# Kernel tuning notes

Hardware: AMD Instinct MI355X
Metric: run time of the kernel (lower is better)

## Reference

```python
import jax, jax.numpy as jnp
import numpy as np

E = 1024
H = 16
HD = E // H
D = 8  # lattice.d
B, S = 4, 1024


def setup_inputs() -> dict:
    key = jax.random.key(0)
    ks = jax.random.split(key, 9)
    inp = {
        'input_encodings': jax.random.normal(ks[0], (B, S, E, D), dtype=jnp.float32),
        'q_weight_encodings': jax.random.normal(ks[1], (E, E, D), dtype=jnp.float32) * 0.02,
        'k_weight_encodings': jax.random.normal(ks[2], (E, E, D), dtype=jnp.float32) * 0.02,
        'v_weight_encodings': jax.random.normal(ks[3], (E, E, D), dtype=jnp.float32) * 0.02,
        'out_weight_encodings': jax.random.normal(ks[4], (E, E, D), dtype=jnp.float32) * 0.02,
        'q_bias': jax.random.normal(ks[5], (E,), dtype=jnp.float32),
        'k_bias': jax.random.normal(ks[6], (E,), dtype=jnp.float32),
        'v_bias': jax.random.normal(ks[7], (E,), dtype=jnp.float32),
        'out_bias': jax.random.normal(ks[8], (E,), dtype=jnp.float32),
    }
    return inp


def vlut_matmul(x_enc, w_enc):
    # x_enc: [N, E, d] lattice-encoded activations; w_enc: [E, F, d] lattice-encoded weights.
    # vLUT matrix-multiply = sum over channels of encoded inner products.
    return jnp.einsum('ned,efd->nf', x_enc, w_enc)


def reference(input_encodings, q_weight_encodings, k_weight_encodings, v_weight_encodings,
              out_weight_encodings, q_bias, k_bias, v_bias, out_bias):
    b, s, e, d = input_encodings.shape
    x = input_encodings.reshape(b * s, e, d)

    q = vlut_matmul(x, q_weight_encodings) + q_bias
    k = vlut_matmul(x, k_weight_encodings) + k_bias
    v = vlut_matmul(x, v_weight_encodings) + v_bias

    # [B, H, S, HD]
    q = q.reshape(b, s, H, HD).transpose(0, 2, 1, 3)
    k = k.reshape(b, s, H, HD).transpose(0, 2, 1, 3)
    v = v.reshape(b, s, H, HD).transpose(0, 2, 1, 3)

    scale = 1.0 / np.sqrt(HD).astype(np.float32)
    attn_scores = jnp.einsum('bhqd,bhkd->bhqk', q, k) * scale
    attn_weights = jax.nn.softmax(attn_scores, axis=-1)
    attn_output = jnp.einsum('bhqk,bhkd->bhqd', attn_weights, v)
    attn_output = attn_output.transpose(0, 2, 1, 3).reshape(b * s, e)

    # output vLUT projection (broadcast interpretation over lattice dim d)
    output = jnp.einsum('ne,efd->nf', attn_output, out_weight_encodings)
    output = output.reshape(b, s, e) + out_bias
    return output, attn_weights
```

## Files before the change

### kernel.cpp

```cpp
#include <hip/hip_runtime.h>

typedef _Float16 f16;
typedef f16 f16x8 __attribute__((ext_vector_type(8)));
typedef float f32x4 __attribute__((ext_vector_type(4)));

#define NTOK 4096
#define EDIM 1024
#define KQKV 8192
#define SEQ  1024
#define HD   64

__device__ __forceinline__ float dot4(f32x4 a, f32x4 b) {
  return a[0]*b[0] + a[1]*b[1] + a[2]*b[2] + a[3]*b[3];
}

__device__ __forceinline__ void gl16(const void* g, void* l) {
  __builtin_amdgcn_global_load_lds(
      (const __attribute__((address_space(1))) void*)g,
      (__attribute__((address_space(3))) void*)l, 16, 0, 0);
}

__global__ void k_split(const float* __restrict__ in, f16* __restrict__ hi,
                        f16* __restrict__ lo, int n8) {
  int stride = gridDim.x * blockDim.x;
  for (int i = blockIdx.x * blockDim.x + threadIdx.x; i < n8; i += stride) {
    const float4* p = (const float4*)in + (size_t)i * 2;
    float4 a = p[0], b = p[1];
    float v[8] = {a.x, a.y, a.z, a.w, b.x, b.y, b.z, b.w};
    f16x8 h, l;
#pragma unroll
    for (int j = 0; j < 8; j++) {
      f16 hv = (f16)v[j];
      h[j] = hv;
      l[j] = (f16)(v[j] - (float)hv);
    }
    ((f16x8*)hi)[i] = h;
    ((f16x8*)lo)[i] = l;
  }
}

__global__ void k_wsumt(const float* __restrict__ wout, float* __restrict__ wsumT) {
  __shared__ float tile[32][65];
  int e0 = blockIdx.x * 32, f0 = blockIdx.y * 64;
  int t = threadIdx.x;
#pragma unroll
  for (int rep = 0; rep < 8; rep++) {
    int idx = rep * 256 + t;
    int el = idx >> 6, fl = idx & 63;
    const float* p = wout + ((size_t)(e0 + el) * 1024 + (f0 + fl)) * 8;
    float4 r0 = *(const float4*)p, r1 = *(const float4*)(p + 4);
    tile[el][fl] = r0.x + r0.y + r0.z + r0.w + r1.x + r1.y + r1.z + r1.w;
  }
  __syncthreads();
#pragma unroll
  for (int rep = 0; rep < 8; rep++) {
    int idx = rep * 256 + t;
    int fl = idx >> 5, el = idx & 31;
    wsumT[(size_t)(f0 + fl) * 1024 + (e0 + el)] = tile[el][fl];
  }
}

__global__ __launch_bounds__(256, 2)
void k_gemm_qkv(const f16* __restrict__ xhi, const f16* __restrict__ xlo,
                const f16* __restrict__ wqh, const f16* __restrict__ wql,
                const f16* __restrict__ wkh, const f16* __restrict__ wkl,
                const f16* __restrict__ wvh, const f16* __restrict__ wvl,
                const float* __restrict__ qb, const float* __restrict__ kb,
                const float* __restrict__ vb,
                float* __restrict__ Q, float* __restrict__ K, float* __restrict__ V) {
  __shared__ __align__(16) f16 lAh[4096];
  __shared__ __align__(16) f16 lAl[4096];
  __shared__ __align__(16) f16 lBh[4096];
  __shared__ __align__(16) f16 lBl[4096];

  int z = blockIdx.z;
  const f16* bh_ = z == 0 ? wqh : (z == 1 ? wkh : wvh);
  const f16* bl_ = z == 0 ? wql : (z == 1 ? wkl : wvl);
  const float* bias = z == 0 ? qb : (z == 1 ? kb : vb);
  float* out = z == 0 ? Q : (z == 1 ? K : V);

  int t = threadIdx.x;
  int wave = t >> 6, lane = t & 63;
  int lr = lane & 15, lk = lane >> 4;
  int wr = wave >> 1, wc = wave & 1;
  int rowblk = blockIdx.x * 128, colblk = blockIdx.y * 128;

  {
  }
  int arow = t >> 2, acs = t & 3;
  int agc = acs ^ ((arow >> 1) & 3);
  const f16* pAh = xhi + (size_t)(rowblk + arow) * KQKV + (agc << 3);
  const f16* pAl = xlo + (size_t)(rowblk + arow) * KQKV + (agc << 3);
  const f16* pBh = bh_ + (size_t)(t >> 7) * 8192 + ((size_t)colblk + (t & 127)) * 8;
  const f16* pBl = bl_ + (size_t)(t >> 7) * 8192 + ((size_t)colblk + (t & 127)) * 8;

  f16* dAh0 = lAh + t * 8;            f16* dAh1 = lAh + (t + 256) * 8;
  f16* dAl0 = lAl + t * 8;            f16* dAl1 = lAl + (t + 256) * 8;
  f16* dBh0 = lBh + t * 8;            f16* dBh1 = lBh + (t + 256) * 8;
  f16* dBl0 = lBl + t * 8;            f16* dBl1 = lBl + (t + 256) * 8;

  int aswz = (lk ^ ((lr >> 1) & 3)) << 3;
  int aidx[4];
#pragma unroll
  for (int m = 0; m < 4; m++) aidx[m] = (wr * 64 + m * 16 + lr) * 32 + aswz;
  int bidx[4];
#pragma unroll
  for (int n = 0; n < 4; n++) bidx[n] = (lk * 128 + wc * 64 + n * 16 + lr) << 3;

  f32x4 acc[4][4] = {};

  for (int kt = 0; kt < KQKV / 32; ++kt) {
    gl16(pAh, dAh0);  gl16(pAh + 64 * KQKV, dAh1);
    gl16(pAl, dAl0);  gl16(pAl + 64 * KQKV, dAl1);
    gl16(pBh, dBh0);  gl16(pBh + 2 * 8192, dBh1);
    gl16(pBl, dBl0);  gl16(pBl + 2 * 8192, dBl1);
    pAh += 32; pAl += 32; pBh += 4 * 8192; pBl += 4 * 8192;

    __syncthreads();

    f16x8 ah[4], al[4], bh[4], bl[4];
#pragma unroll
    for (int m = 0; m < 4; m++) {
      ah[m] = *(const f16x8*)&lAh[aidx[m]];
      al[m] = *(const f16x8*)&lAl[aidx[m]];
    }
#pragma unroll
    for (int n = 0; n < 4; n++) {
      bh[n] = *(const f16x8*)&lBh[bidx[n]];
      bl[n] = *(const f16x8*)&lBl[bidx[n]];
    }
#pragma unroll
    for (int m = 0; m < 4; m++)
#pragma unroll
      for (int n = 0; n < 4; n++) {
        acc[m][n] = __builtin_amdgcn_mfma_f32_16x16x32_f16(ah[m], bh[n], acc[m][n], 0, 0, 0);
        acc[m][n] = __builtin_amdgcn_mfma_f32_16x16x32_f16(ah[m], bl[n], acc[m][n], 0, 0, 0);
        acc[m][n] = __builtin_amdgcn_mfma_f32_16x16x32_f16(al[m], bh[n], acc[m][n], 0, 0, 0);
      }

    __syncthreads();
  }

  int row0 = rowblk + wr * 64, col0 = colblk + wc * 64;
  float bv[4];
#pragma unroll
  for (int n = 0; n < 4; n++) bv[n] = bias[col0 + n * 16 + lr];
#pragma unroll
  for (int m = 0; m < 4; m++) {
    int r0 = row0 + m * 16 + lk * 4;
#pragma unroll
    for (int n = 0; n < 4; n++) {
      int c = col0 + n * 16 + lr;
      float* dst = out + (size_t)r0 * EDIM + c;
#pragma unroll
      for (int i = 0; i < 4; i++)
        dst[(size_t)i * EDIM] = acc[m][n][i] + bv[n];
    }
  }
}

__global__ __launch_bounds__(256)
void k_scores(const float* __restrict__ Q, const float* __restrict__ K,
              float* __restrict__ attn) {
  __shared__ float Qt[64][68];
  __shared__ float Kt[64][68];
  int z = blockIdx.z;
  int b = z >> 4, h = z & 15;
  int q0 = blockIdx.x * 64, k0 = blockIdx.y * 64;
  int t = threadIdx.x;
  size_t qbase = ((size_t)(b * SEQ + q0)) * EDIM + h * HD;
  size_t kbase = ((size_t)(b * SEQ + k0)) * EDIM + h * HD;
#pragma unroll
  for (int rep = 0; rep < 4; rep++) {
    int idx = rep * 256 + t;
    int r = idx >> 4, c4 = (idx & 15) * 4;
    *(f32x4*)&Qt[r][c4] = *(const f32x4*)(Q + qbase + (size_t)r * EDIM + c4);
    *(f32x4*)&Kt[r][c4] = *(const f32x4*)(K + kbase + (size_t)r * EDIM + c4);
  }
  __syncthreads();
  int tq = t >> 4, tk = t & 15;
  float acc[4][4] = {};
  for (int c0 = 0; c0 < 64; c0 += 4) {
    f32x4 a4[4], b4[4];
#pragma unroll
    for (int i = 0; i < 4; i++) a4[i] = *(const f32x4*)&Qt[tq + 16 * i][c0];
#pragma unroll
    for (int j = 0; j < 4; j++) b4[j] = *(const f32x4*)&Kt[tk + 16 * j][c0];
#pragma unroll
    for (int i = 0; i < 4; i++)
#pragma unroll
      for (int j = 0; j < 4; j++)
        acc[i][j] += dot4(a4[i], b4[j]);
  }
  const float scale = 0.125f;
  float* dst = attn + ((size_t)z * SEQ + q0) * SEQ + k0;
#pragma unroll
  for (int i = 0; i < 4; i++)
#pragma unroll
    for (int j = 0; j < 4; j++)
      dst[(size_t)(tq + 16 * i) * SEQ + tk + 16 * j] = acc[i][j] * scale;
}

__global__ __launch_bounds__(256)
void k_softmax(float* __restrict__ attn) {
  __shared__ float red[8];
  size_t row = blockIdx.x;
  float* p = attn + row * 1024;
  int t = threadIdx.x;
  float4 v = *(float4*)(p + t * 4);
  float m = fmaxf(fmaxf(v.x, v.y), fmaxf(v.z, v.w));
#pragma unroll
  for (int off = 1; off < 64; off <<= 1) m = fmaxf(m, __shfl_xor(m, off));
  int wv = t >> 6;
  if ((t & 63) == 0) red[wv] = m;
  __syncthreads();
  m = fmaxf(fmaxf(red[0], red[1]), fmaxf(red[2], red[3]));
  float4 e;
  e.x = __expf(v.x - m); e.y = __expf(v.y - m);
  e.z = __expf(v.z - m); e.w = __expf(v.w - m);
  float s = e.x + e.y + e.z + e.w;
#pragma unroll
  for (int off = 1; off < 64; off <<= 1) s += __shfl_xor(s, off);
  if ((t & 63) == 0) red[4 + wv] = s;
  __syncthreads();
  s = red[4] + red[5] + red[6] + red[7];
  float inv = 1.0f / s;
  v.x = e.x * inv; v.y = e.y * inv; v.z = e.z * inv; v.w = e.w * inv;
  *(float4*)(p + t * 4) = v;
}

__global__ __launch_bounds__(256)
void k_pv(const float* __restrict__ attn, const float* __restrict__ V,
          float* __restrict__ aout) {
  __shared__ float Wt[64][68];
  __shared__ float VtT[64][68];
  int z = blockIdx.y;
  int b = z >> 4, h = z & 15;
  int s0 = blockIdx.x * 64;
  int t = threadIdx.x;
  int tq = t >> 4, th = t & 15;
  float acc[4][4] = {};
  for (int k0 = 0; k0 < SEQ; k0 += 64) {
    __syncthreads();
#pragma unroll
    for (int rep = 0; rep < 4; rep++) {
      int idx = rep * 256 + t;
      int r = idx >> 4, c4 = (idx & 15) * 4;
      *(f32x4*)&Wt[r][c4] =
          *(const f32x4*)(attn + ((size_t)z * SEQ + s0 + r) * SEQ + k0 + c4);
      f32x4 vv = *(const f32x4*)(V + ((size_t)(b * SEQ + k0 + r)) * EDIM + h * HD + c4);
#pragma unroll
      for (int c = 0; c < 4; c++) VtT[c4 + c][r] = vv[c];
    }
    __syncthreads();
    for (int c0 = 0; c0 < 64; c0 += 4) {
      f32x4 a4[4], b4[4];
#pragma unroll
      for (int i = 0; i < 4; i++) a4[i] = *(const f32x4*)&Wt[tq + 16 * i][c0];
#pragma unroll
      for (int j = 0; j < 4; j++) b4[j] = *(const f32x4*)&VtT[th + 16 * j][c0];
#pragma unroll
      for (int i = 0; i < 4; i++)
#pragma unroll
        for (int j = 0; j < 4; j++)
          acc[i][j] += dot4(a4[i], b4[j]);
    }
  }
#pragma unroll
  for (int i = 0; i < 4; i++)
#pragma unroll
    for (int j = 0; j < 4; j++)
      aout[((size_t)(b * SEQ + s0 + tq + 16 * i)) * EDIM + h * HD + th + 16 * j] =
          acc[i][j];
}

__global__ __launch_bounds__(256)
void k_outproj(const float* __restrict__ A, const float* __restrict__ BT,
               const float* __restrict__ bias, float* __restrict__ outp) {
  __shared__ float At[64][68];
  __shared__ float Bt[64][68];
  int n0 = blockIdx.x * 64, f0 = blockIdx.y * 64;
  int t = threadIdx.x;
  int tn = t >> 4, tf = t & 15;
  float acc[4][4] = {};
  for (int e0 = 0; e0 < EDIM; e0 += 64) {
    __syncthreads();
#pragma unroll
    for (int rep = 0; rep < 4; rep++) {
      int idx = rep * 256 + t;
      int r = idx >> 4, c4 = (idx & 15) * 4;
      *(f32x4*)&At[r][c4] = *(const f32x4*)(A + (size_t)(n0 + r) * EDIM + e0 + c4);
      *(f32x4*)&Bt[r][c4] = *(const f32x4*)(BT + (size_t)(f0 + r) * EDIM + e0 + c4);
    }
    __syncthreads();
    for (int c0 = 0; c0 < 64; c0 += 4) {
      f32x4 a4[4], b4[4];
#pragma unroll
      for (int i = 0; i < 4; i++) a4[i] = *(const f32x4*)&At[tn + 16 * i][c0];
#pragma unroll
      for (int j = 0; j < 4; j++) b4[j] = *(const f32x4*)&Bt[tf + 16 * j][c0];
#pragma unroll
      for (int i = 0; i < 4; i++)
#pragma unroll
        for (int j = 0; j < 4; j++)
          acc[i][j] += dot4(a4[i], b4[j]);
    }
  }
#pragma unroll
  for (int i = 0; i < 4; i++)
#pragma unroll
    for (int j = 0; j < 4; j++)
      outp[(size_t)(n0 + tn + 16 * i) * EDIM + f0 + tf + 16 * j] =
          acc[i][j] + bias[f0 + tf + 16 * j];
}

extern "C" void kernel_launch(void* const* d_in, const int* in_sizes, int n_in,
                              void* d_out, int out_size, void* d_ws, size_t ws_size,
                              hipStream_t stream) {
  const float* x  = (const float*)d_in[0];
  const float* wq = (const float*)d_in[1];
  const float* wk = (const float*)d_in[2];
  const float* wv = (const float*)d_in[3];
  const float* wo = (const float*)d_in[4];
  const float* qb = (const float*)d_in[5];
  const float* kb = (const float*)d_in[6];
  const float* vb = (const float*)d_in[7];
  const float* ob = (const float*)d_in[8];

  float* outp = (float*)d_out;
  float* attn = outp + (size_t)4 * 1024 * 1024;

  char* w = (char*)d_ws;
  f16* xhi = (f16*)w;  w += (size_t)33554432 * 2;
  f16* xlo = (f16*)w;  w += (size_t)33554432 * 2;
  f16* wqh = (f16*)w;  w += (size_t)8388608 * 2;
  f16* wql = (f16*)w;  w += (size_t)8388608 * 2;
  f16* wkh = (f16*)w;  w += (size_t)8388608 * 2;
  f16* wkl = (f16*)w;  w += (size_t)8388608 * 2;
  f16* wvh = (f16*)w;  w += (size_t)8388608 * 2;
  f16* wvl = (f16*)w;  w += (size_t)8388608 * 2;
  float* Q    = (float*)w; w += (size_t)4194304 * 4;
  float* K    = (float*)w; w += (size_t)4194304 * 4;
  float* V    = (float*)w; w += (size_t)4194304 * 4;
  float* aout = (float*)w; w += (size_t)4194304 * 4;
  float* wsumT = (float*)w; w += (size_t)1048576 * 4;

  k_split<<<8192, 256, 0, stream>>>(x, xhi, xlo, 4194304);
  k_split<<<4096, 256, 0, stream>>>(wq, wqh, wql, 1048576);
  k_split<<<4096, 256, 0, stream>>>(wk, wkh, wkl, 1048576);
  k_split<<<4096, 256, 0, stream>>>(wv, wvh, wvl, 1048576);
  k_wsumt<<<dim3(32, 16), 256, 0, stream>>>(wo, wsumT);
  k_gemm_qkv<<<dim3(32, 8, 3), 256, 0, stream>>>(xhi, xlo, wqh, wql, wkh, wkl,
                                                 wvh, wvl, qb, kb, vb, Q, K, V);
  k_scores<<<dim3(16, 16, 64), 256, 0, stream>>>(Q, K, attn);
  k_softmax<<<65536, 256, 0, stream>>>(attn);
  k_pv<<<dim3(16, 64), 256, 0, stream>>>(attn, V, aout);
  k_outproj<<<dim3(64, 16), 256, 0, stream>>>(aout, wsumT, ob, outp);
}
```

Before: 1.681 ms.

## Fuse scores, softmax and PV into one MFMA attention kernel; MFMA out-projection

Measured after the change: 1.445 ms. 1.16x faster.

```diff
diff --git a/kernel.cpp b/kernel.cpp
--- a/kernel.cpp
+++ b/kernel.cpp
@@ -4,15 +4,10 @@
 typedef f16 f16x8 __attribute__((ext_vector_type(8)));
 typedef float f32x4 __attribute__((ext_vector_type(4)));
 
-#define NTOK 4096
 #define EDIM 1024
 #define KQKV 8192
 #define SEQ  1024
 #define HD   64
-
-__device__ __forceinline__ float dot4(f32x4 a, f32x4 b) {
-  return a[0]*b[0] + a[1]*b[1] + a[2]*b[2] + a[3]*b[3];
-}
 
 __device__ __forceinline__ void gl16(const void* g, void* l) {
   __builtin_amdgcn_global_load_lds(
@@ -39,7 +34,8 @@
   }
 }
 
-__global__ void k_wsumt(const float* __restrict__ wout, float* __restrict__ wsumT) {
+__global__ void k_wsumt(const float* __restrict__ wout, f16* __restrict__ wth,
+                        f16* __restrict__ wtl) {
   __shared__ float tile[32][65];
   int e0 = blockIdx.x * 32, f0 = blockIdx.y * 64;
   int t = threadIdx.x;
@@ -56,7 +52,11 @@
   for (int rep = 0; rep < 8; rep++) {
     int idx = rep * 256 + t;
     int fl = idx >> 5, el = idx & 31;
-    wsumT[(size_t)(f0 + fl) * 1024 + (e0 + el)] = tile[el][fl];
+    float v = tile[el][fl];
+    f16 h = (f16)v;
+    size_t o = (size_t)(f0 + fl) * 1024 + e0 + el;
+    wth[o] = h;
+    wtl[o] = (f16)(v - (float)h);
   }
 }
 
@@ -73,7 +73,7 @@
   __shared__ __align__(16) f16 lBh[4096];
   __shared__ __align__(16) f16 lBl[4096];
 
-  int z = blockIdx.z;
+  int z = blockIdx.y;
   const f16* bh_ = z == 0 ? wqh : (z == 1 ? wkh : wvh);
   const f16* bl_ = z == 0 ? wql : (z == 1 ? wkl : wvl);
   const float* bias = z == 0 ? qb : (z == 1 ? kb : vb);
@@ -83,10 +83,8 @@
   int wave = t >> 6, lane = t & 63;
   int lr = lane & 15, lk = lane >> 4;
   int wr = wave >> 1, wc = wave & 1;
-  int rowblk = blockIdx.x * 128, colblk = blockIdx.y * 128;
-
-  {
-  }
+  int rowblk = blockIdx.z * 128, colblk = blockIdx.x * 128;
+
   int arow = t >> 2, acs = t & 3;
   int agc = acs ^ ((arow >> 1) & 3);
   const f16* pAh = xhi + (size_t)(rowblk + arow) * KQKV + (agc << 3);
@@ -94,10 +92,10 @@
   const f16* pBh = bh_ + (size_t)(t >> 7) * 8192 + ((size_t)colblk + (t & 127)) * 8;
   const f16* pBl = bl_ + (size_t)(t >> 7) * 8192 + ((size_t)colblk + (t & 127)) * 8;
 
-  f16* dAh0 = lAh + t * 8;            f16* dAh1 = lAh + (t + 256) * 8;
-  f16* dAl0 = lAl + t * 8;            f16* dAl1 = lAl + (t + 256) * 8;
-  f16* dBh0 = lBh + t * 8;            f16* dBh1 = lBh + (t + 256) * 8;
-  f16* dBl0 = lBl + t * 8;            f16* dBl1 = lBl + (t + 256) * 8;
+  f16* dAh0 = lAh + t * 8;  f16* dAh1 = lAh + (t + 256) * 8;
+  f16* dAl0 = lAl + t * 8;  f16* dAl1 = lAl + (t + 256) * 8;
+  f16* dBh0 = lBh + t * 8;  f16* dBh1 = lBh + (t + 256) * 8;
+  f16* dBl0 = lBl + t * 8;  f16* dBl1 = lBl + (t + 256) * 8;
 
   int aswz = (lk ^ ((lr >> 1) & 3)) << 3;
   int aidx[4];
@@ -159,159 +157,312 @@
   }
 }
 
+__device__ __forceinline__ void stage_tile64(const float* __restrict__ src,
+                                             f16* __restrict__ dh, f16* __restrict__ dl,
+                                             int sr, int sc4) {
+  const float* p = src + (size_t)sr * EDIM + sc4;
+  float4 v0 = *(const float4*)p;
+  float4 v1 = *(const float4*)(p + 4);
+  float4 v2 = *(const float4*)(p + 8);
+  float4 v3 = *(const float4*)(p + 12);
+  float vv[16] = {v0.x, v0.y, v0.z, v0.w, v1.x, v1.y, v1.z, v1.w,
+                  v2.x, v2.y, v2.z, v2.w, v3.x, v3.y, v3.z, v3.w};
+  f16x8 ha, la, hb, lb;
+#pragma unroll
+  for (int j = 0; j < 8; j++) {
+    f16 x = (f16)vv[j];
+    ha[j] = x; la[j] = (f16)(vv[j] - (float)x);
+    f16 y = (f16)vv[8 + j];
+    hb[j] = y; lb[j] = (f16)(vv[8 + j] - (float)y);
+  }
+  int c0 = sc4 >> 3;
+  int ca = ((c0 ^ (sr & 7)) << 3), cb = (((c0 + 1) ^ (sr & 7)) << 3);
+  *(f16x8*)&dh[sr * 64 + ca] = ha;
+  *(f16x8*)&dl[sr * 64 + ca] = la;
+  *(f16x8*)&dh[sr * 64 + cb] = hb;
+  *(f16x8*)&dl[sr * 64 + cb] = lb;
+}
+
+__device__ __forceinline__ void stage_vt(const float* __restrict__ src,
+                                         f16* __restrict__ dh, f16* __restrict__ dl,
+                                         int sr, int sc4) {
+  const float* p = src + (size_t)sr * EDIM + sc4;
+  float4 v0 = *(const float4*)p;
+  float4 v1 = *(const float4*)(p + 4);
+  float4 v2 = *(const float4*)(p + 8);
+  float4 v3 = *(const float4*)(p + 12);
+  float vv[16] = {v0.x, v0.y, v0.z, v0.w, v1.x, v1.y, v1.z, v1.w,
+                  v2.x, v2.y, v2.z, v2.w, v3.x, v3.y, v3.z, v3.w};
+#pragma unroll
+  for (int j = 0; j < 16; j++) {
+    int hd = sc4 + j;
+    f16 x = (f16)vv[j];
+    int off = hd * 64 + (((sr >> 3) ^ (hd & 7)) << 3) + (sr & 7);
+    dh[off] = x;
+    dl[off] = (f16)(vv[j] - (float)x);
+  }
+}
+
 __global__ __launch_bounds__(256)
-void k_scores(const float* __restrict__ Q, const float* __restrict__ K,
-              float* __restrict__ attn) {
-  __shared__ float Qt[64][68];
-  __shared__ float Kt[64][68];
-  int z = blockIdx.z;
-  int b = z >> 4, h = z & 15;
-  int q0 = blockIdx.x * 64, k0 = blockIdx.y * 64;
-  int t = threadIdx.x;
-  size_t qbase = ((size_t)(b * SEQ + q0)) * EDIM + h * HD;
-  size_t kbase = ((size_t)(b * SEQ + k0)) * EDIM + h * HD;
-#pragma unroll
-  for (int rep = 0; rep < 4; rep++) {
-    int idx = rep * 256 + t;
-    int r = idx >> 4, c4 = (idx & 15) * 4;
-    *(f32x4*)&Qt[r][c4] = *(const f32x4*)(Q + qbase + (size_t)r * EDIM + c4);
-    *(f32x4*)&Kt[r][c4] = *(const f32x4*)(K + kbase + (size_t)r * EDIM + c4);
-  }
-  __syncthreads();
-  int tq = t >> 4, tk = t & 15;
-  float acc[4][4] = {};
-  for (int c0 = 0; c0 < 64; c0 += 4) {
-    f32x4 a4[4], b4[4];
-#pragma unroll
-    for (int i = 0; i < 4; i++) a4[i] = *(const f32x4*)&Qt[tq + 16 * i][c0];
-#pragma unroll
-    for (int j = 0; j < 4; j++) b4[j] = *(const f32x4*)&Kt[tk + 16 * j][c0];
-#pragma unroll
-    for (int i = 0; i < 4; i++)
-#pragma unroll
-      for (int j = 0; j < 4; j++)
-        acc[i][j] += dot4(a4[i], b4[j]);
-  }
-  const float scale = 0.125f;
-  float* dst = attn + ((size_t)z * SEQ + q0) * SEQ + k0;
-#pragma unroll
-  for (int i = 0; i < 4; i++)
-#pragma unroll
-    for (int j = 0; j < 4; j++)
-      dst[(size_t)(tq + 16 * i) * SEQ + tk + 16 * j] = acc[i][j] * scale;
-}
-
-__global__ __launch_bounds__(256)
-void k_softmax(float* __restrict__ attn) {
-  __shared__ float red[8];
-  size_t row = blockIdx.x;
-  float* p = attn + row * 1024;
-  int t = threadIdx.x;
-  float4 v = *(float4*)(p + t * 4);
-  float m = fmaxf(fmaxf(v.x, v.y), fmaxf(v.z, v.w));
-#pragma unroll
-  for (int off = 1; off < 64; off <<= 1) m = fmaxf(m, __shfl_xor(m, off));
-  int wv = t >> 6;
-  if ((t & 63) == 0) red[wv] = m;
-  __syncthreads();
-  m = fmaxf(fmaxf(red[0], red[1]), fmaxf(red[2], red[3]));
-  float4 e;
-  e.x = __expf(v.x - m); e.y = __expf(v.y - m);
-  e.z = __expf(v.z - m); e.w = __expf(v.w - m);
-  float s = e.x + e.y + e.z + e.w;
-#pragma unroll
-  for (int off = 1; off < 64; off <<= 1) s += __shfl_xor(s, off);
-  if ((t & 63) == 0) red[4 + wv] = s;
-  __syncthreads();
-  s = red[4] + red[5] + red[6] + red[7];
-  float inv = 1.0f / s;
-  v.x = e.x * inv; v.y = e.y * inv; v.z = e.z * inv; v.w = e.w * inv;
-  *(float4*)(p + t * 4) = v;
-}
-
-__global__ __launch_bounds__(256)
-void k_pv(const float* __restrict__ attn, const float* __restrict__ V,
-          float* __restrict__ aout) {
-  __shared__ float Wt[64][68];
-  __shared__ float VtT[64][68];
+void k_attn(const float* __restrict__ Qm, const float* __restrict__ Km,
+            const float* __restrict__ Vm, float* __restrict__ attn,
+            f16* __restrict__ aoh, f16* __restrict__ aol) {
+  __shared__ __align__(16) f16 lKh[4096], lKl[4096];
+  __shared__ __align__(16) f16 lVh[4096], lVl[4096];
+  __shared__ __align__(16) f16 lP[4096];
+  __shared__ float sred[4][64], ssum[4][64];
+  __shared__ float m_run[64], l_run[64], linv[64];
+
   int z = blockIdx.y;
   int b = z >> 4, h = z & 15;
-  int s0 = blockIdx.x * 64;
+  int q0 = blockIdx.x * 64;
   int t = threadIdx.x;
-  int tq = t >> 4, th = t & 15;
-  float acc[4][4] = {};
-  for (int k0 = 0; k0 < SEQ; k0 += 64) {
-    __syncthreads();
-#pragma unroll
-    for (int rep = 0; rep < 4; rep++) {
-      int idx = rep * 256 + t;
-      int r = idx >> 4, c4 = (idx & 15) * 4;
-      *(f32x4*)&Wt[r][c4] =
-          *(const f32x4*)(attn + ((size_t)z * SEQ + s0 + r) * SEQ + k0 + c4);
-      f32x4 vv = *(const f32x4*)(V + ((size_t)(b * SEQ + k0 + r)) * EDIM + h * HD + c4);
-#pragma unroll
-      for (int c = 0; c < 4; c++) VtT[c4 + c][r] = vv[c];
-    }
-    __syncthreads();
-    for (int c0 = 0; c0 < 64; c0 += 4) {
-      f32x4 a4[4], b4[4];
-#pragma unroll
-      for (int i = 0; i < 4; i++) a4[i] = *(const f32x4*)&Wt[tq + 16 * i][c0];
-#pragma unroll
-      for (int j = 0; j < 4; j++) b4[j] = *(const f32x4*)&VtT[th + 16 * j][c0];
+  int w = t >> 6, lane = t & 63, lr = lane & 15, lk = lane >> 4;
+
+  size_t qoff = ((size_t)b * SEQ + q0) * EDIM + h * HD;
+  size_t koff = ((size_t)b * SEQ) * EDIM + h * HD;
+  size_t abase = ((size_t)z * SEQ + q0) * SEQ;
+
+  int sr = t >> 2, sc4 = (t & 3) * 16;
+
+  stage_tile64(Qm + qoff, lKh, lKl, sr, sc4);
+  __syncthreads();
+  f16x8 qh[4][2], ql[4][2];
+#pragma unroll
+  for (int m = 0; m < 4; m++)
+#pragma unroll
+    for (int kk = 0; kk < 2; kk++) {
+      int r = m * 16 + lr;
+      int ch = (((kk * 4 + lk) ^ (r & 7)) << 3);
+      qh[m][kk] = *(const f16x8*)&lKh[r * 64 + ch];
+      ql[m][kk] = *(const f16x8*)&lKl[r * 64 + ch];
+    }
+  if (t < 64) { m_run[t] = -1e30f; l_run[t] = 0.f; }
+  __syncthreads();
+
+  for (int kt = 0; kt < 16; kt++) {
+    stage_tile64(Km + koff + (size_t)(kt * 64) * EDIM, lKh, lKl, sr, sc4);
+    __syncthreads();
+
+    f16x8 kbh[2], kbl[2];
+#pragma unroll
+    for (int kk = 0; kk < 2; kk++) {
+      int r = w * 16 + lr;
+      int ch = (((kk * 4 + lk) ^ (r & 7)) << 3);
+      kbh[kk] = *(const f16x8*)&lKh[r * 64 + ch];
+      kbl[kk] = *(const f16x8*)&lKl[r * 64 + ch];
+    }
+    f32x4 acc[4] = {};
+#pragma unroll
+    for (int m = 0; m < 4; m++)
+#pragma unroll
+      for (int kk = 0; kk < 2; kk++) {
+        acc[m] = __builtin_amdgcn_mfma_f32_16x16x32_f16(qh[m][kk], kbh[kk], acc[m], 0, 0, 0);
+        acc[m] = __builtin_amdgcn_mfma_f32_16x16x32_f16(qh[m][kk], kbl[kk], acc[m], 0, 0, 0);
+        acc[m] = __builtin_amdgcn_mfma_f32_16x16x32_f16(ql[m][kk], kbh[kk], acc[m], 0, 0, 0);
+      }
+
+    float sv[4][4], rm[4][4];
+#pragma unroll
+    for (int m = 0; m < 4; m++)
+#pragma unroll
+      for (int i = 0; i < 4; i++) { sv[m][i] = acc[m][i] * 0.125f; rm[m][i] = sv[m][i]; }
+#pragma unroll
+    for (int off = 1; off < 16; off <<= 1)
+#pragma unroll
+      for (int m = 0; m < 4; m++)
+#pragma unroll
+        for (int i = 0; i < 4; i++)
+          rm[m][i] = fmaxf(rm[m][i], __shfl_xor(rm[m][i], off));
+    if (lr == 0) {
+#pragma unroll
+      for (int m = 0; m < 4; m++)
+#pragma unroll
+        for (int i = 0; i < 4; i++) sred[w][m * 16 + lk * 4 + i] = rm[m][i];
+    }
+    __syncthreads();
+    if (t < 64) {
+      float tm = fmaxf(fmaxf(sred[0][t], sred[1][t]), fmaxf(sred[2][t], sred[3][t]));
+      float mn = fmaxf(m_run[t], tm);
+      sred[0][t] = __expf(m_run[t] - mn);
+      m_run[t] = mn;
+    }
+    __syncthreads();
+#pragma unroll
+    for (int m = 0; m < 4; m++)
 #pragma unroll
       for (int i = 0; i < 4; i++)
-#pragma unroll
-        for (int j = 0; j < 4; j++)
-          acc[i][j] += dot4(a4[i], b4[j]);
-    }
-  }
-#pragma unroll
-  for (int i = 0; i < 4; i++)
-#pragma unroll
-    for (int j = 0; j < 4; j++)
-      aout[((size_t)(b * SEQ + s0 + tq + 16 * i)) * EDIM + h * HD + th + 16 * j] =
-          acc[i][j];
-}
-
-__global__ __launch_bounds__(256)
-void k_outproj(const float* __restrict__ A, const float* __restrict__ BT,
+        sv[m][i] = __expf(sv[m][i] - m_run[m * 16 + lk * 4 + i]);
+#pragma unroll
+    for (int off = 1; off < 16; off <<= 1)
+#pragma unroll
+      for (int m = 0; m < 4; m++)
+#pragma unroll
+        for (int i = 0; i < 4; i++)
+          sv[m][i] += __shfl_xor(sv[m][i], off);
+    if (lr == 0) {
+#pragma unroll
+      for (int m = 0; m < 4; m++)
+#pragma unroll
+        for (int i = 0; i < 4; i++) ssum[w][m * 16 + lk * 4 + i] = sv[m][i];
+    }
+    __syncthreads();
+    if (t < 64)
+      l_run[t] = l_run[t] * sred[0][t] +
+                 (ssum[0][t] + ssum[1][t] + ssum[2][t] + ssum[3][t]);
+    __syncthreads();
+  }
+  if (t < 64) linv[t] = 1.0f / l_run[t];
+  __syncthreads();
+
+  f32x4 acc_o[4] = {};
+  for (int kt = 0; kt < 16; kt++) {
+    stage_tile64(Km + koff + (size_t)(kt * 64) * EDIM, lKh, lKl, sr, sc4);
+    stage_vt(Vm + koff + (size_t)(kt * 64) * EDIM, lVh, lVl, sr, sc4);
+    __syncthreads();
+
+    f16x8 kbh[2], kbl[2];
+#pragma unroll
+    for (int kk = 0; kk < 2; kk++) {
+      int r = w * 16 + lr;
+      int ch = (((kk * 4 + lk) ^ (r & 7)) << 3);
+      kbh[kk] = *(const f16x8*)&lKh[r * 64 + ch];
+      kbl[kk] = *(const f16x8*)&lKl[r * 64 + ch];
+    }
+    f32x4 acc[4] = {};
+#pragma unroll
+    for (int m = 0; m < 4; m++)
+#pragma unroll
+      for (int kk = 0; kk < 2; kk++) {
+        acc[m] = __builtin_amdgcn_mfma_f32_16x16x32_f16(qh[m][kk], kbh[kk], acc[m], 0, 0, 0);
+        acc[m] = __builtin_amdgcn_mfma_f32_16x16x32_f16(qh[m][kk], kbl[kk], acc[m], 0, 0, 0);
+        acc[m] = __builtin_amdgcn_mfma_f32_16x16x32_f16(ql[m][kk], kbh[kk], acc[m], 0, 0, 0);
+      }
+
+#pragma unroll
+    for (int m = 0; m < 4; m++)
+#pragma unroll
+      for (int i = 0; i < 4; i++) {
+        int row = m * 16 + lk * 4 + i;
+        float pr = __expf(acc[m][i] * 0.125f - m_run[row]) * linv[row];
+        attn[abase + (size_t)row * SEQ + kt * 64 + w * 16 + lr] = pr;
+        int key = w * 16 + lr;
+        lP[row * 64 + (((key >> 3) ^ (row & 7)) << 3) + (key & 7)] = (f16)pr;
+      }
+    __syncthreads();
+
+#pragma unroll
+    for (int kk = 0; kk < 2; kk++) {
+      int rv = w * 16 + lr;
+      int chv = (((kk * 4 + lk) ^ (rv & 7)) << 3);
+      f16x8 vbh = *(const f16x8*)&lVh[rv * 64 + chv];
+      f16x8 vbl = *(const f16x8*)&lVl[rv * 64 + chv];
+#pragma unroll
+      for (int m = 0; m < 4; m++) {
+        int rp = m * 16 + lr;
+        int chp = (((kk * 4 + lk) ^ (rp & 7)) << 3);
+        f16x8 pa = *(const f16x8*)&lP[rp * 64 + chp];
+        acc_o[m] = __builtin_amdgcn_mfma_f32_16x16x32_f16(pa, vbh, acc_o[m], 0, 0, 0);
+        acc_o[m] = __builtin_amdgcn_mfma_f32_16x16x32_f16(pa, vbl, acc_o[m], 0, 0, 0);
+      }
+    }
+    __syncthreads();
+  }
+
+  size_t obase = ((size_t)b * SEQ + q0) * EDIM + h * HD + w * 16 + lr;
+#pragma unroll
+  for (int m = 0; m < 4; m++)
+#pragma unroll
+    for (int i = 0; i < 4; i++) {
+      int row = m * 16 + lk * 4 + i;
+      float v = acc_o[m][i];
+      f16 hh = (f16)v;
+      aoh[obase + (size_t)row * EDIM] = hh;
+      aol[obase + (size_t)row * EDIM] = (f16)(v - (float)hh);
+    }
+}
+
+__global__ __launch_bounds__(256, 2)
+void k_outproj(const f16* __restrict__ aoh, const f16* __restrict__ aol,
+               const f16* __restrict__ wth, const f16* __restrict__ wtl,
                const float* __restrict__ bias, float* __restrict__ outp) {
-  __shared__ float At[64][68];
-  __shared__ float Bt[64][68];
-  int n0 = blockIdx.x * 64, f0 = blockIdx.y * 64;
+  __shared__ __align__(16) f16 lAh[4096], lAl[4096], lBh[4096], lBl[4096];
+
   int t = threadIdx.x;
-  int tn = t >> 4, tf = t & 15;
-  float acc[4][4] = {};
-  for (int e0 = 0; e0 < EDIM; e0 += 64) {
-    __syncthreads();
-#pragma unroll
-    for (int rep = 0; rep < 4; rep++) {
-      int idx = rep * 256 + t;
-      int r = idx >> 4, c4 = (idx & 15) * 4;
-      *(f32x4*)&At[r][c4] = *(const f32x4*)(A + (size_t)(n0 + r) * EDIM + e0 + c4);
-      *(f32x4*)&Bt[r][c4] = *(const f32x4*)(BT + (size_t)(f0 + r) * EDIM + e0 + c4);
-    }
-    __syncthreads();
-    for (int c0 = 0; c0 < 64; c0 += 4) {
-      f32x4 a4[4], b4[4];
-#pragma unroll
-      for (int i = 0; i < 4; i++) a4[i] = *(const f32x4*)&At[tn + 16 * i][c0];
-#pragma unroll
-      for (int j = 0; j < 4; j++) b4[j] = *(const f32x4*)&Bt[tf + 16 * j][c0];
+  int wave = t >> 6, lane = t & 63;
+  int lr = lane & 15, lk = lane >> 4;
+  int wr = wave >> 1, wc = wave & 1;
+  int rowblk = blockIdx.y * 128, colblk = blockIdx.x * 128;
+
+  int arow = t >> 2, acs = t & 3;
+  int agc = acs ^ ((arow >> 1) & 3);
+  const f16* pAh = aoh + (size_t)(rowblk + arow) * EDIM + (agc << 3);
+  const f16* pAl = aol + (size_t)(rowblk + arow) * EDIM + (agc << 3);
+  const f16* pBh = wth + (size_t)(colblk + arow) * EDIM + (agc << 3);
+  const f16* pBl = wtl + (size_t)(colblk + arow) * EDIM + (agc << 3);
+
+  f16* dAh0 = lAh + t * 8;  f16* dAh1 = lAh + (t + 256) * 8;
+  f16* dAl0 = lAl + t * 8;  f16* dAl1 = lAl + (t + 256) * 8;
+  f16* dBh0 = lBh + t * 8;  f16* dBh1 = lBh + (t + 256) * 8;
+  f16* dBl0 = lBl + t * 8;  f16* dBl1 = lBl + (t + 256) * 8;
+
+  int aswz = (lk ^ ((lr >> 1) & 3)) << 3;
+  int aidx[4], bidx[4];
+#pragma unroll
+  for (int m = 0; m < 4; m++) aidx[m] = (wr * 64 + m * 16 + lr) * 32 + aswz;
+#pragma unroll
+  for (int n = 0; n < 4; n++) bidx[n] = (wc * 64 + n * 16 + lr) * 32 + aswz;
+
+  f32x4 acc[4][4] = {};
+
+  for (int kt = 0; kt < 32; ++kt) {
+    gl16(pAh, dAh0);  gl16(pAh + 64 * EDIM, dAh1);
+    gl16(pAl, dAl0);  gl16(pAl + 64 * EDIM, dAl1);
+    gl16(pBh, dBh0);  gl16(pBh + 64 * EDIM, dBh1);
+    gl16(pBl, dBl0);  gl16(pBl + 64 * EDIM, dBl1);
+    pAh += 32; pAl += 32; pBh += 32; pBl += 32;
+
+    __syncthreads();
+
+    f16x8 ah[4], al[4], bh[4], bl[4];
+#pragma unroll
+    for (int m = 0; m < 4; m++) {
+      ah[m] = *(const f16x8*)&lAh[aidx[m]];
+      al[m] = *(const f16x8*)&lAl[aidx[m]];
+    }
+#pragma unroll
+    for (int n = 0; n < 4; n++) {
+      bh[n] = *(const f16x8*)&lBh[bidx[n]];
+      bl[n] = *(const f16x8*)&lBl[bidx[n]];
+    }
+#pragma unroll
+    for (int m = 0; m < 4; m++)
+#pragma unroll
+      for (int n = 0; n < 4; n++) {
+        acc[m][n] = __builtin_amdgcn_mfma_f32_16x16x32_f16(ah[m], bh[n], acc[m][n], 0, 0, 0);
+        acc[m][n] = __builtin_amdgcn_mfma_f32_16x16x32_f16(ah[m], bl[n], acc[m][n], 0, 0, 0);
+        acc[m][n] = __builtin_amdgcn_mfma_f32_16x16x32_f16(al[m], bh[n], acc[m][n], 0, 0, 0);
+      }
+
+    __syncthreads();
+  }
+
+  int row0 = rowblk + wr * 64, col0 = colblk + wc * 64;
+  float bv[4];
+#pragma unroll
+  for (int n = 0; n < 4; n++) bv[n] = bias[col0 + n * 16 + lr];
+#pragma unroll
+  for (int m = 0; m < 4; m++) {
+    int r0 = row0 + m * 16 + lk * 4;
+#pragma unroll
+    for (int n = 0; n < 4; n++) {
+      int c = col0 + n * 16 + lr;
+      float* dst = outp + (size_t)r0 * EDIM + c;
 #pragma unroll
       for (int i = 0; i < 4; i++)
-#pragma unroll
-        for (int j = 0; j < 4; j++)
-          acc[i][j] += dot4(a4[i], b4[j]);
-    }
-  }
-#pragma unroll
-  for (int i = 0; i < 4; i++)
-#pragma unroll
-    for (int j = 0; j < 4; j++)
-      outp[(size_t)(n0 + tn + 16 * i) * EDIM + f0 + tf + 16 * j] =
-          acc[i][j] + bias[f0 + tf + 16 * j];
+        dst[(size_t)i * EDIM] = acc[m][n][i] + bv[n];
+    }
+  }
 }
 
 extern "C" void kernel_launch(void* const* d_in, const int* in_sizes, int n_in,
@@ -339,21 +490,21 @@
   f16* wkl = (f16*)w;  w += (size_t)8388608 * 2;
   f16* wvh = (f16*)w;  w += (size_t)8388608 * 2;
   f16* wvl = (f16*)w;  w += (size_t)8388608 * 2;
-  float* Q    = (float*)w; w += (size_t)4194304 * 4;
-  float* K    = (float*)w; w += (size_t)4194304 * 4;
-  float* V    = (float*)w; w += (size_t)4194304 * 4;
-  float* aout = (float*)w; w += (size_t)4194304 * 4;
-  float* wsumT = (float*)w; w += (size_t)1048576 * 4;
+  float* Q = (float*)w;   w += (size_t)4194304 * 4;
+  float* K = (float*)w;   w += (size_t)4194304 * 4;
+  float* V = (float*)w;   w += (size_t)4194304 * 4;
+  f16* aoh = (f16*)w;     w += (size_t)4194304 * 2;
+  f16* aol = (f16*)w;     w += (size_t)4194304 * 2;
+  f16* wsth = (f16*)w;    w += (size_t)1048576 * 2;
+  f16* wstl = (f16*)w;    w += (size_t)1048576 * 2;
 
   k_split<<<8192, 256, 0, stream>>>(x, xhi, xlo, 4194304);
   k_split<<<4096, 256, 0, stream>>>(wq, wqh, wql, 1048576);
   k_split<<<4096, 256, 0, stream>>>(wk, wkh, wkl, 1048576);
   k_split<<<4096, 256, 0, stream>>>(wv, wvh, wvl, 1048576);
-  k_wsumt<<<dim3(32, 16), 256, 0, stream>>>(wo, wsumT);
-  k_gemm_qkv<<<dim3(32, 8, 3), 256, 0, stream>>>(xhi, xlo, wqh, wql, wkh, wkl,
+  k_wsumt<<<dim3(32, 16), 256, 0, stream>>>(wo, wsth, wstl);
+  k_gemm_qkv<<<dim3(8, 3, 32), 256, 0, stream>>>(xhi, xlo, wqh, wql, wkh, wkl,
                                                  wvh, wvl, qb, kb, vb, Q, K, V);
-  k_scores<<<dim3(16, 16, 64), 256, 0, stream>>>(Q, K, attn);
-  k_softmax<<<65536, 256, 0, stream>>>(attn);
-  k_pv<<<dim3(16, 64), 256, 0, stream>>>(attn, V, aout);
-  k_outproj<<<dim3(64, 16), 256, 0, stream>>>(aout, wsumT, ob, outp);
-}
+  k_attn<<<dim3(16, 64), 256, 0, stream>>>(Q, K, V, attn, aoh, aol);
+  k_outproj<<<dim3(8, 32), 256, 0, stream>>>(aoh, aol, wsth, wstl, ob, outp);
+}
```
